# Optimization experiments

Measured on AMD Instinct MI355X. Metric: run time of the kernel, lower is better.

The kernel has to match this reference:

```python
import jax, jax.numpy as jnp
import numpy as np

B, T, C = 2, 2048, 1024
H, KH, HD = 16, 4, 64
E, TOPK, I = 8, 2, 1024
GATE = 32
EPS = 1.1920929e-07  # torch F.rms_norm default eps = fp32 machine eps


def rmsnorm(v):
    return v * jax.lax.rsqrt(jnp.mean(v * v, axis=-1, keepdims=True) + EPS)


def rope(v, cos, sin):
    d = v.shape[-1] // 2
    a, b = v[..., :d], v[..., d:]
    return jnp.concatenate([a * cos + b * sin, -a * sin + b * cos], axis=-1)


def setup_inputs() -> dict:
    key = jax.random.key(0)
    ks = jax.random.split(key, 14)
    rn = lambda i, shape, s=1.0: jax.random.normal(ks[i], shape, jnp.float32) * s
    inv_freq = 1.0 / (10000.0 ** (np.arange(HD // 2, dtype=np.float64) / (HD // 2)))
    ang = np.outer(np.arange(T), inv_freq)
    cos = jnp.asarray(np.cos(ang), jnp.float32)[None, :, None, :]
    sin = jnp.asarray(np.sin(ang), jnp.float32)[None, :, None, :]
    w = 0.02
    return {
        'x': rn(0, (B, T, C)),
        've': rn(1, (B, T, KH * HD)),
        'cos': cos,
        'sin': sin,
        'Wq': rn(2, (C, H * HD), w),
        'Wk': rn(3, (KH * HD, C), w),
        'Wv': rn(4, (KH * HD, C), w),
        'Wo': rn(5, (C, C), w),
        've_gate_W': rn(6, (KH, GATE), w),
        'router_W': rn(7, (E, C), w),
        'balance_bias': jnp.zeros((E,), jnp.float32),
        'shared_fc_W': rn(8, (I, C), w),
        'shared_proj_W': rn(9, (C, I), w),
        'exp_fc_W': rn(10, (E, I, C), w),
        'exp_proj_W': rn(11, (E, C, I), w),
        'window_size': T,
    }


def reference(x, ve, cos, sin, Wq, Wk, Wv, Wo, ve_gate_W, router_W, balance_bias,
              shared_fc_W, shared_proj_W, exp_fc_W, exp_proj_W, window_size):
    # ---- attention branch: x = x + attn(norm(x)) ----
    h = rmsnorm(x)
    q = (h @ Wq.T).reshape(B, T, H, HD)
    k = (h @ Wk.T).reshape(B, T, KH, HD)
    v = (h @ Wv.T).reshape(B, T, KH, HD)
    # value-embedding gate (has_ve true for this layer)
    gate = 2.0 * jax.nn.sigmoid(h[..., :GATE] @ ve_gate_W.T)  # [B,T,KH]
    v = v + gate[..., None] * ve.reshape(B, T, KH, HD)
    q, k = rope(q, cos, sin), rope(k, cos, sin)
    q, k = rmsnorm(q), rmsnorm(k)
    g = H // KH
    kr = jnp.repeat(k, g, axis=2)  # GQA expansion [B,T,H,HD]
    vr = jnp.repeat(v, g, axis=2)
    scores = jnp.einsum('bthd,bshd->bhts', q, kr) / jnp.sqrt(jnp.float32(HD))
    ti = jnp.arange(T)[:, None]
    si = jnp.arange(T)[None, :]
    mask = (si <= ti) & (si > ti - window_size)  # causal + sliding window
    scores = jnp.where(mask, scores, -jnp.inf)
    p = jax.nn.softmax(scores, axis=-1)
    y = jnp.einsum('bhts,bshd->bthd', p, vr).reshape(B, T, C)
    x = x + y @ Wo.T

    # ---- MoE branch: x = x + shared(norm(x)) + routed(norm(x)) ----
    h2 = rmsnorm(x)
    shared = jnp.square(jax.nn.relu(h2 @ shared_fc_W.T)) @ shared_proj_W.T
    flat = h2.reshape(-1, C)  # [N,C]
    logits = flat @ router_W.T  # [N,E]
    sc = jax.nn.sigmoid(logits)
    _, topi = jax.lax.top_k(sc + balance_bias, TOPK)  # select on biased scores
    topw = jnp.take_along_axis(sc, topi, axis=1)      # weights from raw scores
    topw = topw / (jnp.sum(topw, axis=-1, keepdims=True) + 1e-20)
    N = flat.shape[0]
    combine = jnp.zeros((N, E), flat.dtype).at[jnp.arange(N)[:, None], topi].add(topw)
    # dense grouped compute, mathematically equal to gather/scatter dispatch
    he = jnp.square(jax.nn.relu(jnp.einsum('nc,eic->eni', flat, exp_fc_W)))
    oe = jnp.einsum('eni,eci->enc', he, exp_proj_W)
    routed = jnp.einsum('enc,ne->nc', oe, combine).reshape(B, T, C)
    return x + shared + routed
```

## Files before the change

### kernel.cpp

```cpp
#include <hip/hip_runtime.h>

#define TT 2048
#define CC 1024
#define NTOK 4096
#define EPSF 1.1920929e-07f

typedef unsigned short u16;
typedef short bf16x8 __attribute__((ext_vector_type(8)));
typedef u16 u16x4 __attribute__((ext_vector_type(4)));
typedef float f32x4 __attribute__((ext_vector_type(4)));

__device__ __forceinline__ u16 f2b(float f) {
  union { float f; unsigned u; } v; v.f = f;
  unsigned r = v.u + 0x7FFFu + ((v.u >> 16) & 1u);
  return (u16)(r >> 16);
}
__device__ __forceinline__ float b2f(u16 u) {
  union { unsigned u; float f; } v; v.u = ((unsigned)u) << 16;
  return v.f;
}
__device__ __forceinline__ void gload16(const u16* g, u16* l) {
  __builtin_amdgcn_global_load_lds(
      (const __attribute__((address_space(1))) void*)g,
      (__attribute__((address_space(3))) void*)l, 16, 0, 0);
}
__device__ __forceinline__ bf16x8 ldsf(const u16* s, int row, int kseg) {
  return *(const bf16x8*)(s + (row << 6) + ((kseg ^ (row & 7)) << 3));
}

__global__ __launch_bounds__(256) void rmsnorm_split_k(const float* __restrict__ in,
                                                       u16* __restrict__ hio,
                                                       u16* __restrict__ loo,
                                                       const float* __restrict__ gW,
                                                       float* __restrict__ gates,
                                                       const float* __restrict__ p0,
                                                       const float* __restrict__ p1,
                                                       const float* __restrict__ p2,
                                                       const float* __restrict__ p3,
                                                       u16* __restrict__ h0, u16* __restrict__ l0,
                                                       u16* __restrict__ h1, u16* __restrict__ l1,
                                                       u16* __restrict__ h2, u16* __restrict__ l2,
                                                       u16* __restrict__ h3, u16* __restrict__ l3) {
  const int bid = blockIdx.x;
  const int t = threadIdx.x;
  if (bid >= NTOK) {
    int chunk = (bid - NTOK) * 256 + t;
    const float* inw; u16* ho; u16* lo2; int loc;
    if (chunk < 131072)      { inw = p0; ho = h0; lo2 = l0; loc = chunk; }
    else if (chunk < 163840) { inw = p1; ho = h1; lo2 = l1; loc = chunk - 131072; }
    else if (chunk < 196608) { inw = p2; ho = h2; lo2 = l2; loc = chunk - 163840; }
    else                     { inw = p3; ho = h3; lo2 = l3; loc = chunk - 196608; }
    size_t i = (size_t)loc * 8;
    float v[8];
    *(float4*)v = *(const float4*)(inw + i);
    *(float4*)(v + 4) = *(const float4*)(inw + i + 4);
    u16 hh[8], ll[8];
#pragma unroll
    for (int j = 0; j < 8; ++j) {
      hh[j] = f2b(v[j]);
      ll[j] = f2b(v[j] - b2f(hh[j]));
    }
    *(bf16x8*)(ho + i) = *(bf16x8*)hh;
    *(bf16x8*)(lo2 + i) = *(bf16x8*)ll;
    return;
  }
  const int rowi = bid;
  float4 v = ((const float4*)(in + (size_t)rowi * CC))[t];
  float ss = v.x * v.x + v.y * v.y + v.z * v.z + v.w * v.w;
#pragma unroll
  for (int off = 32; off; off >>= 1) ss += __shfl_down(ss, off, 64);
  __shared__ float red[4];
  __shared__ float hshare[32];
  if ((t & 63) == 0) red[t >> 6] = ss;
  __syncthreads();
  float tot = red[0] + red[1] + red[2] + red[3];
  float sc = rsqrtf(tot * (1.0f / CC) + EPSF);
  float o[4] = {v.x * sc, v.y * sc, v.z * sc, v.w * sc};
  u16 h[4], l[4];
#pragma unroll
  for (int j = 0; j < 4; ++j) {
    h[j] = f2b(o[j]);
    l[j] = f2b(o[j] - b2f(h[j]));
  }
  *(u16x4*)(hio + (size_t)rowi * CC + t * 4) = *(u16x4*)h;
  *(u16x4*)(loo + (size_t)rowi * CC + t * 4) = *(u16x4*)l;
  if (t < 8) *(float4*)&hshare[t << 2] = *(float4*)o;
  __syncthreads();
  if (t < 4) {
    const float* gw = gW + (t << 5);
    float dot = 0.f;
#pragma unroll
    for (int j = 0; j < 32; ++j) dot += hshare[j] * gw[j];
    gates[(rowi << 2) + t] = 2.f / (1.f + __expf(-dot));
  }
}

__global__ __launch_bounds__(256) void rmsnorm_logits_k(const float* __restrict__ in,
                                                        u16* __restrict__ b16o,
                                                        const float* __restrict__ rW,
                                                        float* __restrict__ logits) {
  const int rowi = blockIdx.x;
  const int t = threadIdx.x;
  float4 v = ((const float4*)(in + (size_t)rowi * CC))[t];
  float ss = v.x * v.x + v.y * v.y + v.z * v.z + v.w * v.w;
#pragma unroll
  for (int off = 32; off; off >>= 1) ss += __shfl_down(ss, off, 64);
  __shared__ float red[4];
  __shared__ float red2[8][4];
  if ((t & 63) == 0) red[t >> 6] = ss;
  __syncthreads();
  float tot = red[0] + red[1] + red[2] + red[3];
  float sc = rsqrtf(tot * (1.0f / CC) + EPSF);
  float o[4] = {v.x * sc, v.y * sc, v.z * sc, v.w * sc};
  u16 h[4] = {f2b(o[0]), f2b(o[1]), f2b(o[2]), f2b(o[3])};
  *(u16x4*)(b16o + (size_t)rowi * CC + t * 4) = *(u16x4*)h;
  const float* rwp = rW + (t << 2);
  float part[8];
#pragma unroll
  for (int e = 0; e < 8; ++e) {
    const float* w = rwp + (e << 10);
    part[e] = o[0] * w[0] + o[1] * w[1] + o[2] * w[2] + o[3] * w[3];
  }
  const int wid = t >> 6;
#pragma unroll
  for (int e = 0; e < 8; ++e) {
    float p = part[e];
#pragma unroll
    for (int off = 32; off; off >>= 1) p += __shfl_down(p, off, 64);
    if ((t & 63) == 0) red2[e][wid] = p;
  }
  __syncthreads();
  if (t < 8) logits[rowi * 8 + t] = red2[t][0] + red2[t][1] + red2[t][2] + red2[t][3];
}

template <int MODE>
__global__ __launch_bounds__(256) void gemm_bf_k(
    const u16* __restrict__ A, const u16* __restrict__ A2,
    const u16* __restrict__ Wt, const u16* __restrict__ W2,
    const u16* __restrict__ Wk1, const u16* __restrict__ Wk2,
    const u16* __restrict__ Wv1, const u16* __restrict__ Wv2,
    float* __restrict__ Cf, u16* __restrict__ Cb,
    u16* __restrict__ Ck, u16* __restrict__ Cv,
    const float* __restrict__ addv, int N, int K,
    const int* __restrict__ offsets, const int* __restrict__ counts,
    const int* __restrict__ tok_idx, const float* __restrict__ tok_w,
    const float* __restrict__ cosb, const float* __restrict__ sinb,
    const float* __restrict__ gates, const float* __restrict__ vein) {
  constexpr bool SPLIT = (MODE == 6 || MODE == 11);
  __shared__ __align__(16) u16 Asw[SPLIT ? 16384 : 8192];
  __shared__ __align__(16) u16 Bsw[SPLIT ? 8192 : 4096];
  const int t = threadIdx.x;
  const int lane = t & 63;
  const int l15 = lane & 15, hi = lane >> 4;
  const int wave = t >> 6;
  const int e = blockIdx.z;
  const int mt = blockIdx.y << 7;
  const int bn = blockIdx.x << 6;
  int base = 0, cnt = 0;
  if (MODE == 4 || MODE == 5) {
    cnt = (e == 8) ? NTOK : counts[e];
    if (mt >= cnt) return;
    base = (e == 8) ? 8192 : offsets[e];
  }
  const int r8 = t >> 3;
  const int ksg = (t & 7) ^ (r8 & 7);
  const u16* asrc[4];
  const u16* bsrc[2];
  const u16* asrc2[4];
  const u16* bsrc2[2];
  const u16* W1p = Wt;
  if (MODE == 4 || MODE == 5) W1p = (e == 8) ? Wk1 : Wt + ((size_t)e << 20);
  const u16* W2p = W2;
  int wrow = bn;
  if (MODE == 11) {
    if (bn >= 1280)      { W1p = Wv1; W2p = Wv2; wrow = bn - 1280; }
    else if (bn >= 1024) { W1p = Wk1; W2p = Wk2; wrow = bn - 1024; }
  }
#pragma unroll
  for (int g = 0; g < 4; ++g) {
    int rl = (g << 5) + r8;
    int arow;
    if (MODE == 4) {
      int rr = mt + rl; if (rr > cnt - 1) rr = cnt - 1;
      arow = (e == 8) ? rr : tok_idx[base + rr];
    } else if (MODE == 5) {
      int rr = mt + rl; if (rr > cnt - 1) rr = cnt - 1;
      arow = base + rr;
    } else {
      arow = mt + rl;
    }
    size_t ao = (size_t)arow * K + (ksg << 3);
    asrc[g] = A + ao;
    if (SPLIT) asrc2[g] = A2 + ao;
  }
#pragma unroll
  for (int g = 0; g < 2; ++g) {
    size_t bo = (size_t)(wrow + (g << 5) + r8) * K + (ksg << 3);
    bsrc[g] = W1p + bo;
    if (SPLIT) bsrc2[g] = W2p + bo;
  }
  f32x4 acc[2][4] = {};
  const int nkt = K >> 6;
  for (int kt = 0; kt < nkt; ++kt) {
    __syncthreads();
    const int ko = kt << 6;
#pragma unroll
    for (int g = 0; g < 4; ++g) {
      int co = ((g << 8) + t) << 3;
      gload16(asrc[g] + ko, &Asw[co]);
      if (SPLIT) gload16(asrc2[g] + ko, &Asw[8192 + co]);
    }
#pragma unroll
    for (int g = 0; g < 2; ++g) {
      int co = ((g << 8) + t) << 3;
      gload16(bsrc[g] + ko, &Bsw[co]);
      if (SPLIT) gload16(bsrc2[g] + ko, &Bsw[4096 + co]);
    }
    __syncthreads();
#pragma unroll
    for (int kk = 0; kk < 2; ++kk) {
      bf16x8 ah[2], bh[4];
#pragma unroll
      for (int mi = 0; mi < 2; ++mi)
        ah[mi] = ldsf(Asw, (wave << 5) + (mi << 4) + l15, (kk << 2) + hi);
#pragma unroll
      for (int nj = 0; nj < 4; ++nj)
        bh[nj] = ldsf(Bsw, (nj << 4) + l15, (kk << 2) + hi);
#pragma unroll
      for (int mi = 0; mi < 2; ++mi)
#pragma unroll
        for (int nj = 0; nj < 4; ++nj)
          acc[mi][nj] = __builtin_amdgcn_mfma_f32_16x16x32_bf16(ah[mi], bh[nj], acc[mi][nj], 0, 0, 0);
      if (SPLIT) {
        bf16x8 al[2], bl[4];
#pragma unroll
        for (int mi = 0; mi < 2; ++mi)
          al[mi] = ldsf(Asw + 8192, (wave << 5) + (mi << 4) + l15, (kk << 2) + hi);
#pragma unroll
        for (int nj = 0; nj < 4; ++nj)
          bl[nj] = ldsf(Bsw + 4096, (nj << 4) + l15, (kk << 2) + hi);
#pragma unroll
        for (int mi = 0; mi < 2; ++mi)
#pragma unroll
          for (int nj = 0; nj < 4; ++nj) {
            acc[mi][nj] = __builtin_amdgcn_mfma_f32_16x16x32_bf16(ah[mi], bl[nj], acc[mi][nj], 0, 0, 0);
            acc[mi][nj] = __builtin_amdgcn_mfma_f32_16x16x32_bf16(al[mi], bh[nj], acc[mi][nj], 0, 0, 0);
          }
      }
    }
  }
  if (MODE == 11) {
    if (bn < 1280) {
      u16* outp = (bn < 1024) ? Cb : Ck;
      const int stride = (bn < 1024) ? 1024 : 256;
      const int cbase = (bn < 1024) ? bn : (bn - 1024);
#pragma unroll
      for (int mi = 0; mi < 2; ++mi) {
#pragma unroll
        for (int r = 0; r < 4; ++r) {
          int row = mt + (wave << 5) + (mi << 4) + (hi << 2) + r;
          int tpos = row & (TT - 1);
          const float* cp = cosb + (tpos << 5);
          const float* sp = sinb + (tpos << 5);
          float c0 = cp[l15], s0 = sp[l15];
          float c1 = cp[16 + l15], s1 = sp[16 + l15];
          float a0 = acc[mi][0][r], a1 = acc[mi][1][r];
          float b0 = acc[mi][2][r], b1 = acc[mi][3][r];
          float r00 = a0 * c0 + b0 * s0;
          float r01 = a1 * c1 + b1 * s1;
          float r10 = b0 * c0 - a0 * s0;
          float r11 = b1 * c1 - a1 * s1;
          float ss = r00 * r00 + r01 * r01 + r10 * r10 + r11 * r11;
          ss += __shfl_xor(ss, 1, 64); ss += __shfl_xor(ss, 2, 64);
          ss += __shfl_xor(ss, 4, 64); ss += __shfl_xor(ss, 8, 64);
          float scn = rsqrtf(ss * (1.f / 64.f) + EPSF);
          u16* qp = outp + (size_t)row * stride + cbase;
          qp[l15]      = f2b(r00 * scn);
          qp[16 + l15] = f2b(r01 * scn);
          qp[32 + l15] = f2b(r10 * scn);
          qp[48 + l15] = f2b(r11 * scn);
        }
      }
    } else {
      const int cbase = bn - 1280;
      const int kvh = cbase >> 6;
#pragma unroll
      for (int mi = 0; mi < 2; ++mi) {
#pragma unroll
        for (int r = 0; r < 4; ++r) {
          int row = mt + (wave << 5) + (mi << 4) + (hi << 2) + r;
          float g = gates[(row << 2) + kvh];
          const float* vep = vein + ((size_t)row << 8) + cbase;
          size_t vb_base = ((size_t)(((row >> 11) << 2) + kvh) << 17) + (row & (TT - 1));
#pragma unroll
          for (int nj = 0; nj < 4; ++nj) {
            int d = (nj << 4) + l15;
            Cv[vb_base + ((size_t)d << 11)] = f2b(acc[mi][nj][r] + g * vep[d]);
          }
        }
      }
    }
    return;
  }
#pragma unroll
  for (int mi = 0; mi < 2; ++mi) {
#pragma unroll
    for (int r = 0; r < 4; ++r) {
      int rl = (wave << 5) + (mi << 4) + (hi << 2) + r;
      if (MODE == 4 || MODE == 5) {
        int rr = mt + rl;
        if (rr >= cnt) continue;
        if (MODE == 4) {
          size_t ro = (size_t)(base + rr) * N;
#pragma unroll
          for (int nj = 0; nj < 4; ++nj) {
            float v = acc[mi][nj][r];
            v = v > 0.f ? v * v : 0.f;
            Cb[ro + bn + (nj << 4) + l15] = f2b(v);
          }
        } else {
          int tok = (e == 8) ? rr : tok_idx[base + rr];
          float w = (e == 8) ? 1.0f : tok_w[base + rr];
          size_t ro = (size_t)tok * N;
#pragma unroll
          for (int nj = 0; nj < 4; ++nj)
            atomicAdd(&Cf[ro + bn + (nj << 4) + l15], acc[mi][nj][r] * w);
        }
      } else {
        size_t ro = (size_t)(mt + rl) * N;
        float* outp = (float*)Cb;
#pragma unroll
        for (int nj = 0; nj < 4; ++nj) {
          int col = bn + (nj << 4) + l15;
          float v = acc[mi][nj][r] + addv[ro + col];
          Cf[ro + col] = v;
          outp[ro + col] = v;
        }
      }
    }
  }
}

__global__ __launch_bounds__(256) void attn_mfma_k(const u16* __restrict__ qb,
                                                   const u16* __restrict__ kb,
                                                   const u16* __restrict__ vbT,
                                                   u16* __restrict__ yh,
                                                   u16* __restrict__ yl,
                                                   const int* __restrict__ wszp,
                                                   float* __restrict__ po,
                                                   float* __restrict__ pml,
                                                   const float* __restrict__ cSfc,
                                                   const float* __restrict__ cSproj,
                                                   const float* __restrict__ cEfc,
                                                   const float* __restrict__ cEproj,
                                                   u16* __restrict__ oSfc,
                                                   u16* __restrict__ oSproj,
                                                   u16* __restrict__ oEfc,
                                                   u16* __restrict__ oEproj) {
  const int z = blockIdx.z;
  const int b = z >> 1, seg = z & 1;
  const int kvh = blockIdx.y;
  const int qf = 127 - (int)blockIdx.x;
  const int t = threadIdx.x;
  if (qf < 64 && seg) {
    const int cid = (((b << 2) + kvh) << 6) + ((int)blockIdx.x - 64);
    int chunk = cid * 4608 + t;
#pragma unroll
    for (int it = 0; it < 18; ++it, chunk += 256) {
      const float* in;
      u16* ou;
      int loc;
      if (chunk < 131072)       { in = cSfc;   ou = oSfc;   loc = chunk; }
      else if (chunk < 262144)  { in = cSproj; ou = oSproj; loc = chunk - 131072; }
      else if (chunk < 1310720) { in = cEfc;   ou = oEfc;   loc = chunk - 262144; }
      else                      { in = cEproj; ou = oEproj; loc = chunk - 1310720; }
      size_t i = (size_t)loc * 8;
      float4 a = *(const float4*)(in + i);
      float4 bb = *(const float4*)(in + i + 4);
      u16 r[8] = {f2b(a.x), f2b(a.y), f2b(a.z), f2b(a.w),
                  f2b(bb.x), f2b(bb.y), f2b(bb.z), f2b(bb.w)};
      *(bf16x8*)(ou + i) = *(bf16x8*)r;
    }
    return;
  }
  const int Wn = *wszp;
  const int lane = t & 63, wave = t >> 6;
  const int h = (kvh << 2) + wave;
  const int l15 = lane & 15, hi = lane >> 4;

  __shared__ __align__(16) u16 Klds[2 * 4096];
  __shared__ __align__(16) u16 Vt[2 * 4096];
  __shared__ __align__(16) u16 Plds[4][16 * 64];

  const int qrow0 = qf << 4;
  const int diag = qrow0 >> 6;
  int lo = qrow0 - Wn + 1;
  const int kt0f = lo > 0 ? (lo >> 6) : 0;
  int kt0 = kt0f, ktend = diag;
  if (qf >= 64) {
    int nt = diag - kt0f + 1;
    int mid = kt0f + (nt >> 1);
    if (seg == 0) ktend = mid - 1; else kt0 = mid;
  }

  bf16x8 aQ0, aQ1;
  {
    const u16* qp = qb + ((size_t)((b << 11) + qrow0 + l15) << 10) + (h << 6) + (hi << 3);
    aQ0 = *(const bf16x8*)qp;
    aQ1 = *(const bf16x8*)(qp + 32);
  }
  f32x4 o[4] = {};
  float mrow[4] = {-INFINITY, -INFINITY, -INFINITY, -INFINITY};
  float lrow[4] = {0.f, 0.f, 0.f, 0.f};

  const int kr0 = t >> 3, kc = t & 7;
  const u16* vbase = vbT + ((size_t)((b << 2) + kvh) << 17);

#pragma unroll
  for (int i = 0; i < 2; ++i) {
    int row = kr0 + (i << 5);
    int scol = (kc ^ (row & 7)) << 3;
    gload16(kb + ((size_t)((b << 11) + (kt0 << 6) + row) << 8) + (kvh << 6) + scol,
            &Klds[(t << 3) + (i << 11)]);
    gload16(vbase + ((size_t)row << 11) + (kt0 << 6) + scol,
            &Vt[(t << 3) + (i << 11)]);
  }
  int cur = 0;

  for (int kt = kt0; kt <= ktend; ++kt) {
    __syncthreads();
    if (kt + 1 <= ktend) {
      const int nb = (cur ^ 1) << 12;
#pragma unroll
      for (int i = 0; i < 2; ++i) {
        int row = kr0 + (i << 5);
        int scol = (kc ^ (row & 7)) << 3;
        gload16(kb + ((size_t)((b << 11) + ((kt + 1) << 6) + row) << 8) + (kvh << 6) + scol,
                &Klds[nb + (t << 3) + (i << 11)]);
        gload16(vbase + ((size_t)row << 11) + ((kt + 1) << 6) + scol,
                &Vt[nb + (t << 3) + (i << 11)]);
      }
    }
    const u16* Kb = Klds + (cur << 12);
    const u16* Vb = Vt + (cur << 12);

    float sv[4][4];
    __builtin_amdgcn_s_setprio(1);
#pragma unroll
    for (int kb4 = 0; kb4 < 4; ++kb4) {
      f32x4 S = {0.f, 0.f, 0.f, 0.f};
      bf16x8 B0 = ldsf(Kb, (kb4 << 4) + l15, hi);
      bf16x8 B1 = ldsf(Kb, (kb4 << 4) + l15, 4 + hi);
      S = __builtin_amdgcn_mfma_f32_16x16x32_bf16(aQ0, B0, S, 0, 0, 0);
      S = __builtin_amdgcn_mfma_f32_16x16x32_bf16(aQ1, B1, S, 0, 0, 0);
#pragma unroll
      for (int r = 0; r < 4; ++r) sv[kb4][r] = S[r] * 0.125f;
    }
    __builtin_amdgcn_s_setprio(0);
    if (kt == diag || kt == kt0f) {
#pragma unroll
      for (int kb4 = 0; kb4 < 4; ++kb4) {
        int key = (kt << 6) + (kb4 << 4) + l15;
#pragma unroll
        for (int r = 0; r < 4; ++r) {
          int qg = qrow0 + (hi << 2) + r;
          if (!(key <= qg && key > qg - Wn)) sv[kb4][r] = -INFINITY;
        }
      }
    }

    float scl[4], pv[4][4];
#pragma unroll
    for (int r = 0; r < 4; ++r) {
      float mt2 = fmaxf(fmaxf(sv[0][r], sv[1][r]), fmaxf(sv[2][r], sv[3][r]));
      mt2 = fmaxf(mt2, __shfl_xor(mt2, 1, 64));
      mt2 = fmaxf(mt2, __shfl_xor(mt2, 2, 64));
      mt2 = fmaxf(mt2, __shfl_xor(mt2, 4, 64));
      mt2 = fmaxf(mt2, __shfl_xor(mt2, 8, 64));
      float mn = fmaxf(fmaxf(mrow[r], mt2), -1e30f);
      float sc = __expf(mrow[r] - mn);
      float rs = 0.f;
#pragma unroll
      for (int kb4 = 0; kb4 < 4; ++kb4) {
        float p = __expf(sv[kb4][r] - mn);
        pv[kb4][r] = p;
        rs += p;
      }
      rs += __shfl_xor(rs, 1, 64);
      rs += __shfl_xor(rs, 2, 64);
      rs += __shfl_xor(rs, 4, 64);
      rs += __shfl_xor(rs, 8, 64);
      mrow[r] = mn;
      lrow[r] = lrow[r] * sc + rs;
      scl[r] = sc;
    }

#pragma unroll
    for (int kb4 = 0; kb4 < 4; ++kb4)
#pragma unroll
      for (int r = 0; r < 4; ++r) {
        int row16 = (hi << 2) + r;
        int seg2 = (kb4 << 1) + (l15 >> 3);
        Plds[wave][(row16 << 6) + ((seg2 ^ (row16 & 7)) << 3) + (l15 & 7)] = f2b(pv[kb4][r]);
      }
#pragma unroll
    for (int df = 0; df < 4; ++df) {
      f32x4 t4 = o[df];
      t4[0] *= scl[0]; t4[1] *= scl[1]; t4[2] *= scl[2]; t4[3] *= scl[3];
      o[df] = t4;
    }
    __builtin_amdgcn_s_setprio(1);
#pragma unroll
    for (int ks = 0; ks < 2; ++ks) {
      bf16x8 Ap = ldsf(Plds[wave], l15, (ks << 2) + hi);
#pragma unroll
      for (int df = 0; df < 4; ++df) {
        bf16x8 Bv = ldsf(Vb, (df << 4) + l15, (ks << 2) + hi);
        o[df] = __builtin_amdgcn_mfma_f32_16x16x32_bf16(Ap, Bv, o[df], 0, 0, 0);
      }
    }
    __builtin_amdgcn_s_setprio(0);
    cur ^= 1;
  }

  if (qf < 64) {
    float inv[4];
#pragma unroll
    for (int r = 0; r < 4; ++r) inv[r] = lrow[r] > 0.f ? 1.f / lrow[r] : 0.f;
#pragma unroll
    for (int r = 0; r < 4; ++r) {
      size_t rbase = ((size_t)((b << 11) + qrow0 + (hi << 2) + r) << 10) + (h << 6) + l15;
#pragma unroll
      for (int df = 0; df < 4; ++df) {
        float fo = o[df][r] * inv[r];
        u16 hv = f2b(fo);
        yh[rbase + (df << 4)] = hv;
        yl[rbase + (df << 4)] = f2b(fo - b2f(hv));
      }
    }
  } else {
    const int sidx = (b << 1) + seg;
    const int prow0 = qrow0 - 1024;
#pragma unroll
    for (int r = 0; r < 4; ++r) {
      size_t pbase = ((size_t)(sidx * 1024 + prow0 + (hi << 2) + r) << 10) + (h << 6) + l15;
#pragma unroll
      for (int df = 0; df < 4; ++df) po[pbase + (df << 4)] = o[df][r];
    }
    if (l15 == 0) {
#pragma unroll
      for (int r = 0; r < 4; ++r) {
        size_t mb = ((size_t)(sidx * 1024 + prow0 + (hi << 2) + r) << 5) + (h << 1);
        pml[mb] = mrow[r];
        pml[mb + 1] = lrow[r];
      }
    }
  }
}

__global__ __launch_bounds__(256) void combine_k(const float* __restrict__ po,
                                                 const float* __restrict__ pml,
                                                 u16* __restrict__ yh,
                                                 u16* __restrict__ yl) {
  const int prow = blockIdx.x, b = blockIdx.y;
  const int t = threadIdx.x;
  const int h = t >> 4, d0 = (t & 15) << 2;
  const int s0 = b << 1, s1 = s0 + 1;
  size_t i0 = ((size_t)(s0 * 1024 + prow) << 5) + (h << 1);
  size_t i1 = ((size_t)(s1 * 1024 + prow) << 5) + (h << 1);
  float m0 = pml[i0], l0 = pml[i0 + 1];
  float m1 = pml[i1], l1 = pml[i1 + 1];
  float m = fmaxf(m0, m1);
  float sc0 = __expf(m0 - m), sc1 = __expf(m1 - m);
  float l = l0 * sc0 + l1 * sc1;
  float inv = l > 0.f ? 1.f / l : 0.f;
  size_t o0 = ((size_t)(s0 * 1024 + prow) << 10) + (h << 6) + d0;
  size_t o1 = ((size_t)(s1 * 1024 + prow) << 10) + (h << 6) + d0;
  float4 a = *(const float4*)&po[o0];
  float4 c = *(const float4*)&po[o1];
  float y0 = (a.x * sc0 + c.x * sc1) * inv;
  float y1 = (a.y * sc0 + c.y * sc1) * inv;
  float y2 = (a.z * sc0 + c.z * sc1) * inv;
  float y3 = (a.w * sc0 + c.w * sc1) * inv;
  u16 hv[4] = {f2b(y0), f2b(y1), f2b(y2), f2b(y3)};
  u16 lv[4] = {f2b(y0 - b2f(hv[0])), f2b(y1 - b2f(hv[1])),
               f2b(y2 - b2f(hv[2])), f2b(y3 - b2f(hv[3]))};
  size_t rbase = ((size_t)((b << 11) + 1024 + prow) << 10) + (h << 6) + d0;
  *(u16x4*)(yh + rbase) = *(u16x4*)hv;
  *(u16x4*)(yl + rbase) = *(u16x4*)lv;
}

__global__ __launch_bounds__(256) void topk_k(const float* __restrict__ logits,
                                              const float* __restrict__ bias,
                                              int* __restrict__ topi,
                                              float* __restrict__ topw,
                                              int* __restrict__ counts) {
  int n = blockIdx.x * 256 + threadIdx.x;
  if (n >= NTOK) return;
  float sc[8], sel[8];
#pragma unroll
  for (int e2 = 0; e2 < 8; ++e2) {
    float sg = 1.f / (1.f + __expf(-logits[n * 8 + e2]));
    sc[e2] = sg;
    sel[e2] = sg + bias[e2];
  }
  int i1 = 0; float b1 = sel[0];
#pragma unroll
  for (int j = 1; j < 8; ++j) if (sel[j] > b1) { b1 = sel[j]; i1 = j; }
  int i2 = -1; float b2 = -INFINITY;
#pragma unroll
  for (int j = 0; j < 8; ++j) if (j != i1 && sel[j] > b2) { b2 = sel[j]; i2 = j; }
  float w1 = sc[i1], w2 = sc[i2];
  float invs = 1.f / (w1 + w2 + 1e-20f);
  topi[n * 2] = i1; topi[n * 2 + 1] = i2;
  topw[n * 2] = w1 * invs; topw[n * 2 + 1] = w2 * invs;
  atomicAdd(&counts[i1], 1);
  atomicAdd(&counts[i2], 1);
}

__global__ void scan_k(const int* __restrict__ counts, int* __restrict__ offsets) {
  if (threadIdx.x == 0 && blockIdx.x == 0) {
    int s = 0;
    for (int e2 = 0; e2 < 8; ++e2) { offsets[e2] = s; s += counts[e2]; }
    offsets[8] = s;
  }
}

__global__ __launch_bounds__(256) void scatter_k(const int* __restrict__ topi,
                                                 const float* __restrict__ topw,
                                                 const int* __restrict__ offsets,
                                                 int* __restrict__ counts2,
                                                 int* __restrict__ tok_idx,
                                                 float* __restrict__ tok_w) {
  int n = blockIdx.x * 256 + threadIdx.x;
  if (n >= NTOK) return;
  for (int kk = 0; kk < 2; ++kk) {
    int e2 = topi[n * 2 + kk];
    int slot = atomicAdd(&counts2[e2], 1);
    int p = offsets[e2] + slot;
    tok_idx[p] = n;
    tok_w[p] = topw[n * 2 + kk];
  }
}

extern "C" void kernel_launch(void* const* d_in, const int* in_sizes, int n_in,
                              void* d_out, int out_size, void* d_ws, size_t ws_size,
                              hipStream_t stream) {
  const float* x = (const float*)d_in[0];
  const float* ve = (const float*)d_in[1];
  const float* cosb = (const float*)d_in[2];
  const float* sinb = (const float*)d_in[3];
  const float* Wq = (const float*)d_in[4];
  const float* Wk = (const float*)d_in[5];
  const float* Wv = (const float*)d_in[6];
  const float* Wo = (const float*)d_in[7];
  const float* gW = (const float*)d_in[8];
  const float* routerW = (const float*)d_in[9];
  const float* bias = (const float*)d_in[10];
  const float* Wsfc = (const float*)d_in[11];
  const float* Wsproj = (const float*)d_in[12];
  const float* Wefc = (const float*)d_in[13];
  const float* Weproj = (const float*)d_in[14];
  const int* wsz = (const int*)d_in[15];
  float* out = (float*)d_out;
  char* WS = (char*)d_ws;

  u16* Wefc_b   = (u16*)(WS + 0);
  u16* Weproj_b = (u16*)(WS + 16777216);
  u16* Wsfc_b   = (u16*)(WS + 33554432);
  u16* Wsproj_b = (u16*)(WS + 35651584);
  u16* Wq_hi    = (u16*)(WS + 37748736);
  u16* Wq_lo    = (u16*)(WS + 39845888);
  u16* Wk_hi    = (u16*)(WS + 41943040);
  u16* Wk_lo    = (u16*)(WS + 42467328);
  u16* Wv_hi    = (u16*)(WS + 42991616);
  u16* Wv_lo    = (u16*)(WS + 43515904);
  u16* Wo_hi    = (u16*)(WS + 44040192);
  u16* Wo_lo    = (u16*)(WS + 46137344);
  u16* h_hi     = (u16*)(WS + 48234496);
  u16* h_lo     = (u16*)(WS + 56623104);
  u16* qb       = (u16*)(WS + 65011712);
  u16* kb       = (u16*)(WS + 73400320);
  u16* vb       = (u16*)(WS + 75497472);
  u16* y_hi     = (u16*)(WS + 77594624);
  u16* y_lo     = (u16*)(WS + 85983232);
  float* po     = (float*)(WS + 48234496);
  float* x2     = (float*)(WS + 48234496);
  u16* h2_b     = (u16*)(WS + 85983232);
  u16* he_b     = (u16*)(WS + 48234496);
  float* gates  = (float*)(WS + 94371840);
  float* logits = (float*)(WS + 94437376);
  int* meta     = (int*)(WS + 94568448);
  int* counts   = meta;
  int* counts2  = meta + 8;
  int* offsets  = meta + 16;
  int* topi     = meta + 32;
  float* topw   = (float*)(meta + 8224);
  int* tok_idx  = meta + 16416;
  float* tok_w  = (float*)(meta + 24608);
  float* pml    = (float*)(WS + 94703616);

  hipMemsetAsync(counts, 0, 16 * sizeof(int), stream);

  rmsnorm_split_k<<<NTOK + 1280, 256, 0, stream>>>(x, h_hi, h_lo, gW, gates,
      Wq, Wk, Wv, Wo,
      Wq_hi, Wq_lo, Wk_hi, Wk_lo, Wv_hi, Wv_lo, Wo_hi, Wo_lo);
  gemm_bf_k<11><<<dim3(24, 32), 256, 0, stream>>>(
      h_hi, h_lo, Wq_hi, Wq_lo, Wk_hi, Wk_lo, Wv_hi, Wv_lo,
      nullptr, qb, kb, vb, nullptr, 1536, 1024,
      nullptr, nullptr, nullptr, nullptr, cosb, sinb, gates, ve);
  attn_mfma_k<<<dim3(128, 4, 4), 256, 0, stream>>>(qb, kb, vb, y_hi, y_lo, wsz, po, pml,
      Wsfc, Wsproj, Wefc, Weproj, Wsfc_b, Wsproj_b, Wefc_b, Weproj_b);
  combine_k<<<dim3(1024, 2), 256, 0, stream>>>(po, pml, y_hi, y_lo);
  gemm_bf_k<6><<<dim3(16, 32), 256, 0, stream>>>(
      y_hi, y_lo, Wo_hi, Wo_lo, nullptr, nullptr, nullptr, nullptr,
      x2, (u16*)out, nullptr, nullptr, x, 1024, 1024,
      nullptr, nullptr, nullptr, nullptr, nullptr, nullptr, nullptr, nullptr);
  rmsnorm_logits_k<<<NTOK, 256, 0, stream>>>(x2, h2_b, routerW, logits);
  topk_k<<<16, 256, 0, stream>>>(logits, bias, topi, topw, counts);
  scan_k<<<1, 64, 0, stream>>>(counts, offsets);
  scatter_k<<<16, 256, 0, stream>>>(topi, topw, offsets, counts2, tok_idx, tok_w);
  gemm_bf_k<4><<<dim3(16, 32, 9), 256, 0, stream>>>(
      h2_b, nullptr, Wefc_b, nullptr, Wsfc_b, nullptr, nullptr, nullptr,
      nullptr, he_b, nullptr, nullptr, nullptr, 1024, 1024,
      offsets, counts, tok_idx, nullptr, nullptr, nullptr, nullptr, nullptr);
  gemm_bf_k<5><<<dim3(16, 32, 9), 256, 0, stream>>>(
      he_b, nullptr, Weproj_b, nullptr, Wsproj_b, nullptr, nullptr, nullptr,
      out, nullptr, nullptr, nullptr, nullptr, 1024, 1024,
      offsets, counts, tok_idx, tok_w, nullptr, nullptr, nullptr, nullptr);
}
```

Measured before the change: 388.9 us.

## Fuse router top-k, scan and scatter into one single-block kernel

Replaces the memset plus three routing kernels (top-k with global atomics, serial scan, scatter) with one single-workgroup kernel. It counts per-expert tokens with shared-memory atomics, computes offsets, then recomputes the top-k to scatter token indices and weights. This removes three launches and a memset at the cost of running routing on one workgroup with redundant sigmoid work. It also remaps blockIdx.z in the expert GEMMs so the dense shared-expert slice (e=8) is dispatched first, likely to improve tail balance.

```diff
diff --git a/kernel.cpp b/kernel.cpp
--- a/kernel.cpp
+++ b/kernel.cpp
@@ -153,7 +153,9 @@
   const int lane = t & 63;
   const int l15 = lane & 15, hi = lane >> 4;
   const int wave = t >> 6;
-  const int e = blockIdx.z;
+  const int e = (MODE == 4 || MODE == 5)
+                    ? ((blockIdx.z == 0) ? 8 : (int)blockIdx.z - 1)
+                    : (int)blockIdx.z;
   const int mt = blockIdx.y << 7;
   const int bn = blockIdx.x << 6;
   int base = 0, cnt = 0;
@@ -590,56 +592,63 @@
   *(u16x4*)(yl + rbase) = *(u16x4*)lv;
 }
 
-__global__ __launch_bounds__(256) void topk_k(const float* __restrict__ logits,
-                                              const float* __restrict__ bias,
-                                              int* __restrict__ topi,
-                                              float* __restrict__ topw,
-                                              int* __restrict__ counts) {
-  int n = blockIdx.x * 256 + threadIdx.x;
-  if (n >= NTOK) return;
-  float sc[8], sel[8];
-#pragma unroll
-  for (int e2 = 0; e2 < 8; ++e2) {
-    float sg = 1.f / (1.f + __expf(-logits[n * 8 + e2]));
-    sc[e2] = sg;
-    sel[e2] = sg + bias[e2];
-  }
-  int i1 = 0; float b1 = sel[0];
-#pragma unroll
-  for (int j = 1; j < 8; ++j) if (sel[j] > b1) { b1 = sel[j]; i1 = j; }
-  int i2 = -1; float b2 = -INFINITY;
-#pragma unroll
-  for (int j = 0; j < 8; ++j) if (j != i1 && sel[j] > b2) { b2 = sel[j]; i2 = j; }
-  float w1 = sc[i1], w2 = sc[i2];
-  float invs = 1.f / (w1 + w2 + 1e-20f);
-  topi[n * 2] = i1; topi[n * 2 + 1] = i2;
-  topw[n * 2] = w1 * invs; topw[n * 2 + 1] = w2 * invs;
-  atomicAdd(&counts[i1], 1);
-  atomicAdd(&counts[i2], 1);
-}
-
-__global__ void scan_k(const int* __restrict__ counts, int* __restrict__ offsets) {
-  if (threadIdx.x == 0 && blockIdx.x == 0) {
+__global__ __launch_bounds__(256) void router_all_k(const float* __restrict__ logits,
+                                                    const float* __restrict__ bias,
+                                                    int* __restrict__ counts,
+                                                    int* __restrict__ offsets,
+                                                    int* __restrict__ tok_idx,
+                                                    float* __restrict__ tok_w) {
+  __shared__ int cnt[8], off[9], cnt2[8];
+  const int t = threadIdx.x;
+  if (t < 8) { cnt[t] = 0; cnt2[t] = 0; }
+  __syncthreads();
+  for (int k = 0; k < 16; ++k) {
+    int n = t * 16 + k;
+    float sel[8];
+#pragma unroll
+    for (int e2 = 0; e2 < 8; ++e2)
+      sel[e2] = 1.f / (1.f + __expf(-logits[n * 8 + e2])) + bias[e2];
+    int i1 = 0; float b1 = sel[0];
+#pragma unroll
+    for (int j = 1; j < 8; ++j) if (sel[j] > b1) { b1 = sel[j]; i1 = j; }
+    int i2 = -1; float b2 = -INFINITY;
+#pragma unroll
+    for (int j = 0; j < 8; ++j) if (j != i1 && sel[j] > b2) { b2 = sel[j]; i2 = j; }
+    atomicAdd(&cnt[i1], 1);
+    atomicAdd(&cnt[i2], 1);
+  }
+  __syncthreads();
+  if (t == 0) {
     int s = 0;
-    for (int e2 = 0; e2 < 8; ++e2) { offsets[e2] = s; s += counts[e2]; }
-    offsets[8] = s;
-  }
-}
-
-__global__ __launch_bounds__(256) void scatter_k(const int* __restrict__ topi,
-                                                 const float* __restrict__ topw,
-                                                 const int* __restrict__ offsets,
-                                                 int* __restrict__ counts2,
-                                                 int* __restrict__ tok_idx,
-                                                 float* __restrict__ tok_w) {
-  int n = blockIdx.x * 256 + threadIdx.x;
-  if (n >= NTOK) return;
-  for (int kk = 0; kk < 2; ++kk) {
-    int e2 = topi[n * 2 + kk];
-    int slot = atomicAdd(&counts2[e2], 1);
-    int p = offsets[e2] + slot;
-    tok_idx[p] = n;
-    tok_w[p] = topw[n * 2 + kk];
+    for (int e2 = 0; e2 < 8; ++e2) { off[e2] = s; offsets[e2] = s; counts[e2] = cnt[e2]; s += cnt[e2]; }
+    off[8] = s; offsets[8] = s;
+  }
+  __syncthreads();
+  for (int k = 0; k < 16; ++k) {
+    int n = t * 16 + k;
+    float sc[8], sel[8];
+#pragma unroll
+    for (int e2 = 0; e2 < 8; ++e2) {
+      float sg = 1.f / (1.f + __expf(-logits[n * 8 + e2]));
+      sc[e2] = sg;
+      sel[e2] = sg + bias[e2];
+    }
+    int i1 = 0; float b1 = sel[0];
+#pragma unroll
+    for (int j = 1; j < 8; ++j) if (sel[j] > b1) { b1 = sel[j]; i1 = j; }
+    int i2 = -1; float b2 = -INFINITY;
+#pragma unroll
+    for (int j = 0; j < 8; ++j) if (j != i1 && sel[j] > b2) { b2 = sel[j]; i2 = j; }
+    float w1 = sc[i1], w2 = sc[i2];
+    float invs = 1.f / (w1 + w2 + 1e-20f);
+    int s1 = atomicAdd(&cnt2[i1], 1);
+    int p1 = off[i1] + s1;
+    tok_idx[p1] = n;
+    tok_w[p1] = w1 * invs;
+    int s2 = atomicAdd(&cnt2[i2], 1);
+    int p2 = off[i2] + s2;
+    tok_idx[p2] = n;
+    tok_w[p2] = w2 * invs;
   }
 }
 
@@ -692,15 +701,10 @@
   float* logits = (float*)(WS + 94437376);
   int* meta     = (int*)(WS + 94568448);
   int* counts   = meta;
-  int* counts2  = meta + 8;
   int* offsets  = meta + 16;
-  int* topi     = meta + 32;
-  float* topw   = (float*)(meta + 8224);
   int* tok_idx  = meta + 16416;
   float* tok_w  = (float*)(meta + 24608);
   float* pml    = (float*)(WS + 94703616);
-
-  hipMemsetAsync(counts, 0, 16 * sizeof(int), stream);
 
   rmsnorm_split_k<<<NTOK + 1280, 256, 0, stream>>>(x, h_hi, h_lo, gW, gates,
       Wq, Wk, Wv, Wo,
@@ -717,9 +721,7 @@
       x2, (u16*)out, nullptr, nullptr, x, 1024, 1024,
       nullptr, nullptr, nullptr, nullptr, nullptr, nullptr, nullptr, nullptr);
   rmsnorm_logits_k<<<NTOK, 256, 0, stream>>>(x2, h2_b, routerW, logits);
-  topk_k<<<16, 256, 0, stream>>>(logits, bias, topi, topw, counts);
-  scan_k<<<1, 64, 0, stream>>>(counts, offsets);
-  scatter_k<<<16, 256, 0, stream>>>(topi, topw, offsets, counts2, tok_idx, tok_w);
+  router_all_k<<<1, 256, 0, stream>>>(logits, bias, counts, offsets, tok_idx, tok_w);
   gemm_bf_k<4><<<dim3(16, 32, 9), 256, 0, stream>>>(
       h2_b, nullptr, Wefc_b, nullptr, Wsfc_b, nullptr, nullptr, nullptr,
       nullptr, he_b, nullptr, nullptr, nullptr, 1024, 1024,
```

Result: faster. 320.4 us (-17.6%).
